# Kernel tuning notes

Measured on AMD Instinct MI355X. Metric: run time of the kernel, lower is better.

The kernel has to match this reference:

```python
import jax, jax.numpy as jnp
import numpy as np

B, T = 128, 512
IN, Z, H, E, TR = 88, 80, 400, 100, 200


def setup_inputs() -> dict:
    key = jax.random.key(0)
    ks = jax.random.split(key, 16)
    r = lambda i, shape: (0.05 * jax.random.normal(ks[i], shape)).astype(jnp.float32)
    z32 = lambda n: jnp.zeros((n,), dtype=jnp.float32)
    return dict(
        mini_batch=jax.random.uniform(ks[0], (B, T, IN), dtype=jnp.float32),
        eps=jax.random.normal(ks[1], (B, T, Z), dtype=jnp.float32),
        W_ih=r(2, (H, IN)), W_hh=r(3, (H, H)), b_ih=z32(H), b_hh=z32(H),
        h0=z32(H), z0=z32(Z),
        W_loc=r(4, (Z, H)), b_loc=z32(Z), W_scale=r(5, (Z, H)), b_scale=z32(Z),
        gW1=r(6, (TR, Z)), gb1=z32(TR), gW2=r(7, (Z, TR)), gb2=z32(Z),
        pW1=r(8, (TR, Z)), pb1=z32(TR), pW2=r(9, (Z, TR)), pb2=z32(Z),
        sW=r(10, (Z, Z)), sb=z32(Z),
        lW=jnp.eye(Z, dtype=jnp.float32), lb=z32(Z),  # lin_z_to_loc initialized to identity in torch code
        eW1=r(11, (E, Z)), eb1=z32(E), eW2=r(12, (E, E)), eb2=z32(E),
        eW3=r(13, (IN, E)), eb3=z32(IN),
    )


def reference(mini_batch, eps, W_ih, W_hh, b_ih, b_hh, h0, z0,
              W_loc, b_loc, W_scale, b_scale,
              gW1, gb1, gW2, gb2, pW1, pb1, pW2, pb2, sW, sb, lW, lb,
              eW1, eb1, eW2, eb2, eW3, eb3):
    Bb = mini_batch.shape[0]
    # --- guide: Elman RNN (relu) over time-reversed input, then reverse back ---
    xr = mini_batch[:, ::-1, :]                          # [B,T,IN]
    pre = jnp.einsum('bti,hi->bth', xr, W_ih) + b_ih     # [B,T,H] input projection precomputed

    def step(h, p):                                      # h:[B,H], p:[B,H]
        h = jax.nn.relu(p + h @ W_hh.T + b_hh)
        return h, h

    h_init = jnp.broadcast_to(h0, (Bb, h0.shape[0]))
    _, hs = jax.lax.scan(step, h_init, jnp.swapaxes(pre, 0, 1))  # hs:[T,B,H]
    rnn_out = jnp.swapaxes(hs, 0, 1)[:, ::-1, :]         # pad_and_reverse (full-length seqs)

    # --- Combiner (meanfield): q(z_t) params, reparameterized sample ---
    z_loc = rnn_out @ W_loc.T + b_loc                    # [B,T,Z]
    z_scale = jax.nn.softplus(rnn_out @ W_scale.T + b_scale)
    z = z_loc + z_scale * eps                            # rsample

    # --- model: GatedTransition on shifted z ---
    z_shift = jnp.concatenate([jnp.broadcast_to(z0, (Bb, 1, z0.shape[0])), z[:, :-1]], axis=1)
    gate = jax.nn.sigmoid(jax.nn.relu(z_shift @ gW1.T + gb1) @ gW2.T + gb2)
    prop = jax.nn.relu(z_shift @ pW1.T + pb1) @ pW2.T + pb2
    trans_loc = (1.0 - gate) * (z_shift @ lW.T + lb) + gate * prop
    trans_scale = jax.nn.softplus(jax.nn.relu(prop) @ sW.T + sb)

    # --- Emitter: p(x_t | z_t) ---
    h1 = jax.nn.relu(z @ eW1.T + eb1)
    h2 = jax.nn.relu(h1 @ eW2.T + eb2)
    emis = jax.nn.sigmoid(h2 @ eW3.T + eb3)              # [B,T,IN]

    return jnp.concatenate([emis, trans_loc, trans_scale], axis=-1)  # [B,T,IN+2Z]
```

## Files before the change

### kernel.cpp

```cpp
#include <hip/hip_runtime.h>
#include <math.h>

typedef unsigned int uint;

constexpr int BB  = 128;
constexpr int TT  = 512;
constexpr int DIN = 88;
constexpr int DZ  = 80;
constexpr int DH  = 400;
constexpr int DE  = 100;
constexpr int DTR = 200;
constexpr int DOUT = DIN + DZ + DZ;

typedef __attribute__((ext_vector_type(8))) short bf16x8;
typedef __attribute__((ext_vector_type(4))) float f32x4;
union FU { uint4 u; bf16x8 v; };

__device__ __forceinline__ float softplusf(float x) {
    return fmaxf(x, 0.f) + log1pf(__expf(-fabsf(x)));
}
__device__ __forceinline__ float sigmoidf(float x) {
    return 1.f / (1.f + __expf(-x));
}
__device__ __forceinline__ uint bf16rn(float f) {
    uint u = __float_as_uint(f);
    return (u + 0x7FFFu + ((u >> 16) & 1u)) >> 16;
}
__device__ __forceinline__ uint pk2(float lo, float hi) {
    return bf16rn(lo) | (bf16rn(hi) << 16);
}
#define DOT2(ACC, Wv, Hv) asm("v_dot2_f32_bf16 %0, %1, %2, %0" : "+v"(ACC) : "v"(Wv), "v"(Hv))

__device__ __forceinline__ bf16x8 fragF32(const float* p) {
    float4 f0 = *(const float4*)p, f1 = *(const float4*)(p + 4);
    FU fu;
    fu.u.x = pk2(f0.x, f0.y); fu.u.y = pk2(f0.z, f0.w);
    fu.u.z = pk2(f1.x, f1.y); fu.u.w = pk2(f1.z, f1.w);
    return fu.v;
}
__device__ __forceinline__ bf16x8 fragF32relu(const float* p) {
    float4 f0 = *(const float4*)p, f1 = *(const float4*)(p + 4);
    FU fu;
    fu.u.x = pk2(fmaxf(f0.x, 0.f), fmaxf(f0.y, 0.f));
    fu.u.y = pk2(fmaxf(f0.z, 0.f), fmaxf(f0.w, 0.f));
    fu.u.z = pk2(fmaxf(f1.x, 0.f), fmaxf(f1.y, 0.f));
    fu.u.w = pk2(fmaxf(f1.z, 0.f), fmaxf(f1.w, 0.f));
    return fu.v;
}
#define MFMA(A, B, C) __builtin_amdgcn_mfma_f32_16x16x32_bf16((A), (B), (C), 0, 0, 0)


__global__ void packb_kernel(const float* __restrict__ W, uint* __restrict__ dst,
                             int O, int K, int KS, int tileOff) {
    int tile = blockIdx.x, r = threadIdx.x;
    int l = r >> 2, d = r & 3;
    int nt = tile / KS, ks = tile % KS;
    int o = nt * 16 + (l & 15);
    int k = ks * 32 + ((l >> 4) << 3) + 2 * d;
    uint lo = 0, hi = 0;
    if (o < O && k < K)     lo = bf16rn(W[o * K + k]);
    if (o < O && k + 1 < K) hi = bf16rn(W[o * K + k + 1]);
    dst[(size_t)(tileOff + tile) * 256 + r] = lo | (hi << 16);
}

__global__ void pack_rnn(const float* __restrict__ W_hh, uint* __restrict__ Wb) {
    int idx = blockIdx.x * 256 + threadIdx.x;
    if (idx >= 200 * 512) return;
    int t = idx & 511, j = idx >> 9;
    uint val = 0u;
    int p = -1, hf = 0;
    if (t < 200) { p = t; hf = 0; }
    else if (t >= 256 && t < 456) { p = t - 256; hf = 1; }
    if (p >= 0) {
        int r  = 2 * p + (j >= 100 ? 1 : 0);
        int kd = hf * 100 + (j % 100);
        val = pk2(W_hh[r * DH + 2 * kd], W_hh[r * DH + 2 * kd + 1]);
    }
    Wb[(j >> 2) * 2048 + t * 4 + (j & 3)] = val;
}

__global__ __launch_bounds__(256) void pre_kernel(
    const float* __restrict__ x, const uint* __restrict__ bt,
    const float* __restrict__ b_ih, const float* __restrict__ b_hh,
    float* __restrict__ pre) {
    __shared__ float xs[16 * 100];
    const int b = blockIdx.y, tt0 = blockIdx.x * 16, tid = threadIdx.x;
    const int l = tid & 63, wid = tid >> 6, lr = l & 15, lg = l >> 4;
    for (int idx = tid; idx < 1600; idx += 256) {
        int r = idx / 100, k = idx % 100;
        xs[idx] = (k < DIN) ? x[((size_t)b * TT + (TT - 1 - (tt0 + r))) * DIN + k] : 0.f;
    }
    __syncthreads();
    bf16x8 af[3];
    #pragma unroll
    for (int ks = 0; ks < 3; ++ks) af[ks] = fragF32(xs + lr * 100 + ks * 32 + lg * 8);
    const uint4* bt4 = (const uint4*)bt;
    for (int nt = wid; nt < 25; nt += 4) {
        f32x4 acc = {0.f, 0.f, 0.f, 0.f};
        const uint4* bp = bt4 + (size_t)(388 + nt * 3) * 64 + l;
        #pragma unroll
        for (int ks = 0; ks < 3; ++ks) { FU bu; bu.u = bp[ks * 64]; acc = MFMA(af[ks], bu.v, acc); }
        int col = nt * 16 + lr;
        float bias = b_ih[col] + b_hh[col];
        #pragma unroll
        for (int i = 0; i < 4; ++i)
            pre[((size_t)b * TT + tt0 + lg * 4 + i) * DH + col] = acc[i] + bias;
    }
}

#define DLOOP(OFF)                                                              \
    _Pragma("unroll")                                                           \
    for (int d = 0; d < 100; ++d) {                                             \
        const int kd = (OFF) + d;                                               \
        const int hsrc = ((kd >> 6) == 0) ? hl0 : ((kd >> 6) == 1) ? hl1        \
                        : ((kd >> 6) == 2) ? hl2 : hl3;                         \
        int hv = __builtin_amdgcn_readlane(hsrc, kd & 63);                      \
        if (d & 1) { DOT2(r0b, W[d], hv); DOT2(r1b, W[100 + d], hv); }          \
        else       { DOT2(r0a, W[d], hv); DOT2(r1a, W[100 + d], hv); }          \
    }

__global__ __launch_bounds__(512) __attribute__((amdgpu_waves_per_eu(2, 2)))
void rnn_kernel(const uint* __restrict__ Wb, const float* __restrict__ h0,
                float* hs) {
    __shared__ uint h_lds[256];
    __shared__ float2 part[200];

    const int tid = threadIdx.x;
    const int lane = tid & 63;
    const bool a0 = (tid < 200);
    const bool a1 = (tid >= 256) && (tid < 456);
    const int p = a0 ? tid : (a1 ? tid - 256 : 0);

    uint W[200];
    const uint4* Wb4 = (const uint4*)Wb;
    #pragma unroll
    for (int j4 = 0; j4 < 50; ++j4) {
        uint4 v = Wb4[j4 * 512 + tid];
        W[4 * j4 + 0] = v.x; W[4 * j4 + 1] = v.y;
        W[4 * j4 + 2] = v.z; W[4 * j4 + 3] = v.w;
    }
    #pragma unroll
    for (int j = 0; j < 200; ++j) asm volatile("" : "+v"(W[j]));

    if (tid < 256)
        h_lds[tid] = (tid < 200) ? pk2(h0[2 * tid], h0[2 * tid + 1]) : 0u;
    __syncthreads();

    float* base = hs + (size_t)blockIdx.x * TT * DH;
    float2 pcur = make_float2(0.f, 0.f);
    if (a0) pcur = *(const float2*)(base + 2 * p);

    for (int tt = 0; tt < TT; ++tt) {
        int hl0 = (int)h_lds[lane];
        int hl1 = (int)h_lds[64 + lane];
        int hl2 = (int)h_lds[128 + lane];
        int hl3 = (int)h_lds[192 + lane];

        float2 pnxt = make_float2(0.f, 0.f);
        if (a0 && tt + 1 < TT) pnxt = *(const float2*)(base + (size_t)(tt + 1) * DH + 2 * p);

        float r0a = 0.f, r0b = 0.f, r1a = 0.f, r1b = 0.f;
        if (a0)      { DLOOP(0) }
        else if (a1) { DLOOP(100) }

        if (a1) part[p] = make_float2(r0a + r0b, r1a + r1b);
        __syncthreads();
        if (a0) {
            float2 q = part[p];
            float v0 = fmaxf(pcur.x + r0a + r0b + q.x, 0.f);
            float v1 = fmaxf(pcur.y + r1a + r1b + q.y, 0.f);
            uint pkd = pk2(v0, v1);
            h_lds[p] = pkd;
            ((uint*)(base + (size_t)tt * DH))[p] = pkd;
            pcur = pnxt;
        }
        __syncthreads();
    }
}

__global__ __launch_bounds__(256) void e_kernel(
    const uint4* __restrict__ hs4, const float* __restrict__ eps,
    const float* __restrict__ z0, const uint* __restrict__ bt,
    const float* __restrict__ b_loc, const float* __restrict__ b_scale,
    const float* __restrict__ gb1, const float* __restrict__ pb1,
    const float* __restrict__ gb2, const float* __restrict__ pb2,
    const float* __restrict__ lb,  const float* __restrict__ sb,
    const float* __restrict__ eb1, const float* __restrict__ eb2,
    const float* __restrict__ eb3, float* __restrict__ out) {
    __shared__ float lds[12196];
    float* zl = lds;
    float* AP = lds + 1700;
    float* gp = lds + 8996;

    const int tid = threadIdx.x, l = tid & 63, wid = tid >> 6;
    const int b = blockIdx.y, t0 = blockIdx.x * 16;
    const int lr = l & 15, lg = l >> 4;
    const uint4* bt4 = (const uint4*)bt;

    bf16x8 zf[3];

    {
        const int m0 = (wid >> 1) * 16;
        int r = m0 + lr;
        int t = t0 - 1 + r; t = min(max(t, 0), TT - 1);
        const uint4* rp = hs4 + ((size_t)b * TT + (TT - 1 - t)) * 100;
        bf16x8 af[13];
        FU zz; zz.u = make_uint4(0u, 0u, 0u, 0u);
        #pragma unroll
        for (int ks = 0; ks < 13; ++ks) {
            if (ks == 12 && lg >= 2) af[ks] = zz.v;
            else { FU fu; fu.u = rp[ks * 4 + lg]; af[ks] = fu.v; }
        }
        for (int nt = (wid & 1); nt < 10; nt += 2) {
            f32x4 acc = {0.f, 0.f, 0.f, 0.f};
            const uint4* bp = bt4 + (size_t)(nt * 13) * 64 + l;
            #pragma unroll
            for (int ks = 0; ks < 13; ++ks) { FU bu; bu.u = bp[ks * 64]; acc = MFMA(af[ks], bu.v, acc); }
            int col = nt * 16 + lr;
            float bias = (col < DZ) ? b_loc[col] : b_scale[col - DZ];
            #pragma unroll
            for (int i = 0; i < 4; ++i) {
                int rr = m0 + lg * 4 + i;
                if (rr < 17) AP[rr * 164 + col] = acc[i] + bias;
            }
        }
    }
    __syncthreads();

    for (int idx = tid; idx < 17 * 100; idx += 256) {
        int r = idx / 100, o = idx % 100;
        float zv = 0.f;
        if (o < DZ) {
            int t = t0 - 1 + r;
            if (t < 0) zv = z0[o];
            else {
                float sp = softplusf(AP[r * 164 + DZ + o]);
                zv = AP[r * 164 + o] + sp * eps[((size_t)b * TT + t) * DZ + o];
            }
        }
        zl[idx] = zv;
    }
    __syncthreads();

    {
        #pragma unroll
        for (int ks = 0; ks < 3; ++ks) zf[ks] = fragF32(zl + lr * 100 + ks * 32 + lg * 8);
        for (int idx = tid; idx < 640; idx += 256) {
            int h = idx / 320, rem = idx % 320;
            AP[h * 3648 + (rem / 20) * 228 + 208 + rem % 20] = 0.f;
        }
        for (int nt = wid; nt < 26; nt += 4) {
            f32x4 acc = {0.f, 0.f, 0.f, 0.f};
            const uint4* bp = bt4 + (size_t)(130 + nt * 3) * 64 + l;
            #pragma unroll
            for (int ks = 0; ks < 3; ++ks) { FU bu; bu.u = bp[ks * 64]; acc = MFMA(zf[ks], bu.v, acc); }
            int isP = nt >= 13;
            int col = (isP ? nt - 13 : nt) * 16 + lr;
            float bias = (col < DTR) ? (isP ? pb1[col] : gb1[col]) : 0.f;
            float* dst = AP + isP * 3648;
            #pragma unroll
            for (int i = 0; i < 4; ++i)
                dst[(lg * 4 + i) * 228 + col] = fmaxf(acc[i] + bias, 0.f);
        }
    }
    __syncthreads();

    {
        int half = wid >> 1;
        const float* src = AP + half * 3648;
        bf16x8 apf[7];
        #pragma unroll
        for (int ks = 0; ks < 7; ++ks) apf[ks] = fragF32(src + lr * 228 + ks * 32 + lg * 8);
        for (int idx = tid; idx < 640; idx += 256) {
            int h = idx / 320, rem = idx % 320;
            gp[h * 1600 + (rem / 20) * 100 + 80 + rem % 20] = 0.f;
        }
        for (int nt = (wid & 1); nt < 5; nt += 2) {
            f32x4 acc = {0.f, 0.f, 0.f, 0.f};
            const uint4* bp = bt4 + (size_t)(208 + half * 35 + nt * 7) * 64 + l;
            #pragma unroll
            for (int ks = 0; ks < 7; ++ks) { FU bu; bu.u = bp[ks * 64]; acc = MFMA(apf[ks], bu.v, acc); }
            int col = nt * 16 + lr;
            float bias = half ? pb2[col] : gb2[col];
            float* dst = gp + half * 1600;
            #pragma unroll
            for (int i = 0; i < 4; ++i) {
                float v = acc[i] + bias;
                dst[(lg * 4 + i) * 100 + col] = half ? v : sigmoidf(v);
            }
        }
    }
    __syncthreads();

    {
        bf16x8 z1f[3], prf[3];
        #pragma unroll
        for (int ks = 0; ks < 3; ++ks) {
            z1f[ks] = fragF32(zl + (1 + lr) * 100 + ks * 32 + lg * 8);
            prf[ks] = fragF32relu(gp + 1600 + lr * 100 + ks * 32 + lg * 8);
        }
        for (int tsk = wid; tsk < 18; tsk += 4) {
            if (tsk < 5) {
                f32x4 acc = {0.f, 0.f, 0.f, 0.f};
                const uint4* bp = bt4 + (size_t)(278 + tsk * 3) * 64 + l;
                #pragma unroll
                for (int ks = 0; ks < 3; ++ks) { FU bu; bu.u = bp[ks * 64]; acc = MFMA(zf[ks], bu.v, acc); }
                int col = tsk * 16 + lr;
                float bias = lb[col];
                #pragma unroll
                for (int i = 0; i < 4; ++i) {
                    int rr = lg * 4 + i;
                    float g  = gp[rr * 100 + col];
                    float pv = gp[1600 + rr * 100 + col];
                    out[((size_t)b * TT + t0 + rr) * DOUT + DIN + col] =
                        (1.f - g) * (acc[i] + bias) + g * pv;
                }
            } else if (tsk < 10) {
                int nt = tsk - 5;
                f32x4 acc = {0.f, 0.f, 0.f, 0.f};
                const uint4* bp = bt4 + (size_t)(293 + nt * 3) * 64 + l;
                #pragma unroll
                for (int ks = 0; ks < 3; ++ks) { FU bu; bu.u = bp[ks * 64]; acc = MFMA(prf[ks], bu.v, acc); }
                int col = nt * 16 + lr;
                float bias = sb[col];
                #pragma unroll
                for (int i = 0; i < 4; ++i)
                    out[((size_t)b * TT + t0 + lg * 4 + i) * DOUT + DIN + DZ + col] =
                        softplusf(acc[i] + bias);
            } else {
                int nt = tsk - 10;
                f32x4 acc = {0.f, 0.f, 0.f, 0.f};
                const uint4* bp = bt4 + (size_t)(308 + nt * 3) * 64 + l;
                #pragma unroll
                for (int ks = 0; ks < 3; ++ks) { FU bu; bu.u = bp[ks * 64]; acc = MFMA(z1f[ks], bu.v, acc); }
                int col = nt * 16 + lr;
                float bias = (col < DE) ? eb1[col] : 0.f;
                #pragma unroll
                for (int i = 0; i < 4; ++i)
                    AP[(lg * 4 + i) * 228 + col] = fmaxf(acc[i] + bias, 0.f);
            }
        }
    }
    __syncthreads();

    {
        bf16x8 hf[4];
        #pragma unroll
        for (int ks = 0; ks < 4; ++ks) hf[ks] = fragF32(AP + lr * 228 + ks * 32 + lg * 8);
        for (int nt = wid; nt < 8; nt += 4) {
            f32x4 acc = {0.f, 0.f, 0.f, 0.f};
            const uint4* bp = bt4 + (size_t)(332 + nt * 4) * 64 + l;
            #pragma unroll
            for (int ks = 0; ks < 4; ++ks) { FU bu; bu.u = bp[ks * 64]; acc = MFMA(hf[ks], bu.v, acc); }
            int col = nt * 16 + lr;
            float bias = (col < DE) ? eb2[col] : 0.f;
            #pragma unroll
            for (int i = 0; i < 4; ++i)
                AP[3648 + (lg * 4 + i) * 228 + col] = fmaxf(acc[i] + bias, 0.f);
        }
    }
    __syncthreads();

    {
        bf16x8 hf[4];
        #pragma unroll
        for (int ks = 0; ks < 4; ++ks) hf[ks] = fragF32(AP + 3648 + lr * 228 + ks * 32 + lg * 8);
        for (int nt = wid; nt < 6; nt += 4) {
            f32x4 acc = {0.f, 0.f, 0.f, 0.f};
            const uint4* bp = bt4 + (size_t)(364 + nt * 4) * 64 + l;
            #pragma unroll
            for (int ks = 0; ks < 4; ++ks) { FU bu; bu.u = bp[ks * 64]; acc = MFMA(hf[ks], bu.v, acc); }
            int col = nt * 16 + lr;
            if (col < DIN) {
                float bias = eb3[col];
                #pragma unroll
                for (int i = 0; i < 4; ++i)
                    out[((size_t)b * TT + t0 + lg * 4 + i) * DOUT + col] = sigmoidf(acc[i] + bias);
            }
        }
    }
}

extern "C" void kernel_launch(void* const* d_in, const int* in_sizes, int n_in,
                              void* d_out, int out_size, void* d_ws, size_t ws_size,
                              hipStream_t stream) {
    const float* x       = (const float*)d_in[0];
    const float* eps     = (const float*)d_in[1];
    const float* W_ih    = (const float*)d_in[2];
    const float* W_hh    = (const float*)d_in[3];
    const float* b_ih    = (const float*)d_in[4];
    const float* b_hh    = (const float*)d_in[5];
    const float* h0      = (const float*)d_in[6];
    const float* z0      = (const float*)d_in[7];
    const float* W_loc   = (const float*)d_in[8];
    const float* b_loc   = (const float*)d_in[9];
    const float* W_scale = (const float*)d_in[10];
    const float* b_scale = (const float*)d_in[11];
    const float* gW1 = (const float*)d_in[12];
    const float* gb1 = (const float*)d_in[13];
    const float* gW2 = (const float*)d_in[14];
    const float* gb2 = (const float*)d_in[15];
    const float* pW1 = (const float*)d_in[16];
    const float* pb1 = (const float*)d_in[17];
    const float* pW2 = (const float*)d_in[18];
    const float* pb2 = (const float*)d_in[19];
    const float* sW  = (const float*)d_in[20];
    const float* sb  = (const float*)d_in[21];
    const float* lW  = (const float*)d_in[22];
    const float* lb  = (const float*)d_in[23];
    const float* eW1 = (const float*)d_in[24];
    const float* eb1 = (const float*)d_in[25];
    const float* eW2 = (const float*)d_in[26];
    const float* eb2 = (const float*)d_in[27];
    const float* eW3 = (const float*)d_in[28];
    const float* eb3 = (const float*)d_in[29];

    float* wsf = (float*)d_ws;
    float* prebuf = wsf;
    uint*  Wb = (uint*)(wsf + (size_t)BB * TT * DH);
    uint*  bt = Wb + 102400;

    pack_rnn<<<400, 256, 0, stream>>>(W_hh, Wb);
    packb_kernel<<<5 * 13, 256, 0, stream>>>(W_loc,   bt,  DZ, DH, 13, 0);
    packb_kernel<<<5 * 13, 256, 0, stream>>>(W_scale, bt,  DZ, DH, 13, 65);
    packb_kernel<<<13 * 3, 256, 0, stream>>>(gW1,     bt, DTR, DZ,  3, 130);
    packb_kernel<<<13 * 3, 256, 0, stream>>>(pW1,     bt, DTR, DZ,  3, 169);
    packb_kernel<<<5 * 7,  256, 0, stream>>>(gW2,     bt,  DZ, DTR, 7, 208);
    packb_kernel<<<5 * 7,  256, 0, stream>>>(pW2,     bt,  DZ, DTR, 7, 243);
    packb_kernel<<<5 * 3,  256, 0, stream>>>(lW,      bt,  DZ, DZ,  3, 278);
    packb_kernel<<<5 * 3,  256, 0, stream>>>(sW,      bt,  DZ, DZ,  3, 293);
    packb_kernel<<<8 * 3,  256, 0, stream>>>(eW1,     bt,  DE, DZ,  3, 308);
    packb_kernel<<<8 * 4,  256, 0, stream>>>(eW2,     bt,  DE, DE,  4, 332);
    packb_kernel<<<6 * 4,  256, 0, stream>>>(eW3,     bt, DIN, DE,  4, 364);
    packb_kernel<<<25 * 3, 256, 0, stream>>>(W_ih,    bt,  DH, DIN, 3, 388);

    pre_kernel<<<dim3(TT / 16, BB), 256, 0, stream>>>(x, bt, b_ih, b_hh, prebuf);
    rnn_kernel<<<dim3(BB), dim3(512), 0, stream>>>(Wb, h0, prebuf);
    e_kernel<<<dim3(TT / 16, BB), 256, 0, stream>>>(
        (const uint4*)prebuf, eps, z0, bt,
        b_loc, b_scale, gb1, pb1, gb2, pb2, lb, sb, eb1, eb2, eb3,
        (float*)d_out);
}
```

Before: 1.172 ms.

## Batch 16 sequences per block in RNN recurrence using MFMA instead of dot2

The RNN recurrence previously ran one block per sequence (128 blocks), with each thread doing scalar bf16 dot2 products against register-resident W_hh rows. It now runs 8 blocks of 16 sequences each. W_hh is held as MFMA A-fragments in registers, plus one tile in LDS, and the 16 hidden states are multiplied with 16x16x32 bf16 MFMAs each step. Hidden state and pre-activations are double-buffered in LDS so there is one barrier per step, and all weight-packing launches are merged into a single kernel. The trade-off is only 8 CUs active on a serial chain, with heavier register pressure and per-step LDS traffic.

```diff
diff --git a/kernel.cpp b/kernel.cpp
--- a/kernel.cpp
+++ b/kernel.cpp
@@ -14,7 +14,8 @@
 
 typedef __attribute__((ext_vector_type(8))) short bf16x8;
 typedef __attribute__((ext_vector_type(4))) float f32x4;
-union FU { uint4 u; bf16x8 v; };
+typedef __attribute__((ext_vector_type(4))) uint  u32x4;
+union FU { u32x4 u; bf16x8 v; };
 
 __device__ __forceinline__ float softplusf(float x) {
     return fmaxf(x, 0.f) + log1pf(__expf(-fabsf(x)));
@@ -29,8 +30,6 @@
 __device__ __forceinline__ uint pk2(float lo, float hi) {
     return bf16rn(lo) | (bf16rn(hi) << 16);
 }
-#define DOT2(ACC, Wv, Hv) asm("v_dot2_f32_bf16 %0, %1, %2, %0" : "+v"(ACC) : "v"(Wv), "v"(Hv))
-
 __device__ __forceinline__ bf16x8 fragF32(const float* p) {
     float4 f0 = *(const float4*)p, f1 = *(const float4*)(p + 4);
     FU fu;
@@ -49,35 +48,30 @@
 }
 #define MFMA(A, B, C) __builtin_amdgcn_mfma_f32_16x16x32_bf16((A), (B), (C), 0, 0, 0)
 
-
-__global__ void packb_kernel(const float* __restrict__ W, uint* __restrict__ dst,
-                             int O, int K, int KS, int tileOff) {
-    int tile = blockIdx.x, r = threadIdx.x;
-    int l = r >> 2, d = r & 3;
-    int nt = tile / KS, ks = tile % KS;
+struct Srcs { const float* p[13]; };
+
+__global__ __launch_bounds__(256) void packall_kernel(Srcs s, uint* __restrict__ dst) {
+    constexpr int O_[13]   = {80,80,200,200,80,80,80,80,100,100,88,400,400};
+    constexpr int K_[13]   = {400,400,80,80,200,200,80,80,80,100,100,88,400};
+    constexpr int KS_[13]  = {13,13,3,3,7,7,3,3,3,4,4,3,13};
+    constexpr int OFF_[13] = {0,65,130,169,208,243,278,293,308,332,364,388,463};
+    int tile = blockIdx.x;
+    int e = 0;
+    #pragma unroll
+    for (int i = 1; i < 13; ++i) if (tile >= OFF_[i]) e = i;
+    int lt = tile - OFF_[e];
+    int nt = lt / KS_[e], ks = lt % KS_[e];
+    const float* W = s.p[e];
+    int r = threadIdx.x, l = r >> 2, d = r & 3;
     int o = nt * 16 + (l & 15);
     int k = ks * 32 + ((l >> 4) << 3) + 2 * d;
     uint lo = 0, hi = 0;
-    if (o < O && k < K)     lo = bf16rn(W[o * K + k]);
-    if (o < O && k + 1 < K) hi = bf16rn(W[o * K + k + 1]);
-    dst[(size_t)(tileOff + tile) * 256 + r] = lo | (hi << 16);
-}
-
-__global__ void pack_rnn(const float* __restrict__ W_hh, uint* __restrict__ Wb) {
-    int idx = blockIdx.x * 256 + threadIdx.x;
-    if (idx >= 200 * 512) return;
-    int t = idx & 511, j = idx >> 9;
-    uint val = 0u;
-    int p = -1, hf = 0;
-    if (t < 200) { p = t; hf = 0; }
-    else if (t >= 256 && t < 456) { p = t - 256; hf = 1; }
-    if (p >= 0) {
-        int r  = 2 * p + (j >= 100 ? 1 : 0);
-        int kd = hf * 100 + (j % 100);
-        val = pk2(W_hh[r * DH + 2 * kd], W_hh[r * DH + 2 * kd + 1]);
-    }
-    Wb[(j >> 2) * 2048 + t * 4 + (j & 3)] = val;
-}
+    if (o < O_[e] && k < K_[e])     lo = bf16rn(W[o * K_[e] + k]);
+    if (o < O_[e] && k + 1 < K_[e]) hi = bf16rn(W[o * K_[e] + k + 1]);
+    dst[(size_t)tile * 256 + r] = lo | (hi << 16);
+}
+
+constexpr int WHH = 463;
 
 __global__ __launch_bounds__(256) void pre_kernel(
     const float* __restrict__ x, const uint* __restrict__ bt,
@@ -99,7 +93,7 @@
         f32x4 acc = {0.f, 0.f, 0.f, 0.f};
         const uint4* bp = bt4 + (size_t)(388 + nt * 3) * 64 + l;
         #pragma unroll
-        for (int ks = 0; ks < 3; ++ks) { FU bu; bu.u = bp[ks * 64]; acc = MFMA(af[ks], bu.v, acc); }
+        for (int ks = 0; ks < 3; ++ks) { FU bu; bu.u = *(const u32x4*)(bp + ks * 64); acc = MFMA(af[ks], bu.v, acc); }
         int col = nt * 16 + lr;
         float bias = b_ih[col] + b_hh[col];
         #pragma unroll
@@ -108,73 +102,110 @@
     }
 }
 
-#define DLOOP(OFF)                                                              \
-    _Pragma("unroll")                                                           \
-    for (int d = 0; d < 100; ++d) {                                             \
-        const int kd = (OFF) + d;                                               \
-        const int hsrc = ((kd >> 6) == 0) ? hl0 : ((kd >> 6) == 1) ? hl1        \
-                        : ((kd >> 6) == 2) ? hl2 : hl3;                         \
-        int hv = __builtin_amdgcn_readlane(hsrc, kd & 63);                      \
-        if (d & 1) { DOT2(r0b, W[d], hv); DOT2(r1b, W[100 + d], hv); }          \
-        else       { DOT2(r0a, W[d], hv); DOT2(r1a, W[100 + d], hv); }          \
-    }
-
 __global__ __launch_bounds__(512) __attribute__((amdgpu_waves_per_eu(2, 2)))
-void rnn_kernel(const uint* __restrict__ Wb, const float* __restrict__ h0,
-                float* hs) {
-    __shared__ uint h_lds[256];
-    __shared__ float2 part[200];
-
-    const int tid = threadIdx.x;
-    const int lane = tid & 63;
-    const bool a0 = (tid < 200);
-    const bool a1 = (tid >= 256) && (tid < 456);
-    const int p = a0 ? tid : (a1 ? tid - 256 : 0);
-
-    uint W[200];
-    const uint4* Wb4 = (const uint4*)Wb;
+void rnn_kernel(const u32x4* __restrict__ bt4, const float* __restrict__ h0,
+                float* __restrict__ prehs) {
+    extern __shared__ char smem[];
+    uint*  hb   = (uint*)smem;
+    float* pb   = (float*)(smem + 27136);
+    u32x4* wt24 = (u32x4*)(smem + 27136 + 51712);
+
+    const int tid = threadIdx.x, lane = tid & 63, wid = tid >> 6;
+    const int batch = lane & 15, lg = lane >> 4;
+    const int b0 = blockIdx.x * 16;
+
+    u32x4 A0[13], A1[13], A2[13];
+    {
+        const u32x4* base = bt4 + (size_t)(WHH + 3 * wid * 13) * 64 + lane;
+        #pragma unroll
+        for (int ks = 0; ks < 13; ++ks) {
+            A0[ks] = base[ks * 64];
+            A1[ks] = base[(13 + ks) * 64];
+            A2[ks] = base[(26 + ks) * 64];
+        }
+    }
     #pragma unroll
-    for (int j4 = 0; j4 < 50; ++j4) {
-        uint4 v = Wb4[j4 * 512 + tid];
-        W[4 * j4 + 0] = v.x; W[4 * j4 + 1] = v.y;
-        W[4 * j4 + 2] = v.z; W[4 * j4 + 3] = v.w;
-    }
-    #pragma unroll
-    for (int j = 0; j < 200; ++j) asm volatile("" : "+v"(W[j]));
-
-    if (tid < 256)
-        h_lds[tid] = (tid < 200) ? pk2(h0[2 * tid], h0[2 * tid + 1]) : 0u;
-    __syncthreads();
-
-    float* base = hs + (size_t)blockIdx.x * TT * DH;
-    float2 pcur = make_float2(0.f, 0.f);
-    if (a0) pcur = *(const float2*)(base + 2 * p);
-
+    for (int ks = 0; ks < 13; ++ks)
+        asm volatile("" : "+v"(A0[ks]), "+v"(A1[ks]), "+v"(A2[ks]));
+
+    for (int i = tid; i < 13 * 64; i += 512)
+        wt24[i] = bt4[(size_t)(WHH + 24 * 13) * 64 + i];
+
+    for (int i = tid; i < 2 * 16 * 12; i += 512) {
+        int buf = i / 192, r = i % 192, bs = r / 12, d = 200 + r % 12;
+        hb[buf * 3392 + bs * 212 + d] = 0u;
+    }
+    for (int i = tid; i < 16 * 200; i += 512) {
+        int bs = i / 200, d = i % 200;
+        hb[bs * 212 + d] = pk2(h0[2 * d], h0[2 * d + 1]);
+    }
+    {
+        const u32x4* ra = (const u32x4*)(prehs + ((size_t)(b0 + 2 * wid) * TT) * DH);
+        const u32x4* rb = (const u32x4*)(prehs + ((size_t)(b0 + 2 * wid + 1) * TT) * DH);
+        u32x4* wa = (u32x4*)(pb + (2 * wid) * 404);
+        u32x4* wb = (u32x4*)(pb + (2 * wid + 1) * 404);
+        wa[lane] = ra[lane];
+        wb[lane] = rb[lane];
+        if (lane < 36) { wa[64 + lane] = ra[64 + lane]; wb[64 + lane] = rb[64 + lane]; }
+    }
+    __syncthreads();
+
+    uint cur = 0;
     for (int tt = 0; tt < TT; ++tt) {
-        int hl0 = (int)h_lds[lane];
-        int hl1 = (int)h_lds[64 + lane];
-        int hl2 = (int)h_lds[128 + lane];
-        int hl3 = (int)h_lds[192 + lane];
-
-        float2 pnxt = make_float2(0.f, 0.f);
-        if (a0 && tt + 1 < TT) pnxt = *(const float2*)(base + (size_t)(tt + 1) * DH + 2 * p);
-
-        float r0a = 0.f, r0b = 0.f, r1a = 0.f, r1b = 0.f;
-        if (a0)      { DLOOP(0) }
-        else if (a1) { DLOOP(100) }
-
-        if (a1) part[p] = make_float2(r0a + r0b, r1a + r1b);
+        u32x4 na0, na1, nb0, nb1;
+        const bool hasNext = (tt + 1 < TT);
+        if (hasNext) {
+            const u32x4* ra = (const u32x4*)(prehs + ((size_t)(b0 + 2 * wid) * TT + tt + 1) * DH);
+            const u32x4* rb = (const u32x4*)(prehs + ((size_t)(b0 + 2 * wid + 1) * TT + tt + 1) * DH);
+            na0 = ra[lane]; nb0 = rb[lane];
+            if (lane < 36) { na1 = ra[64 + lane]; nb1 = rb[64 + lane]; }
+        }
+
+        const uint*  hcur = hb + cur * 3392;
+        const float* pcur = pb + cur * (16 * 404);
+        f32x4 c0 = {0.f, 0.f, 0.f, 0.f}, c1 = c0, c2 = c0, c24 = c0;
+        const u32x4* hrow = (const u32x4*)(hcur + batch * 212);
+        #pragma unroll
+        for (int ks = 0; ks < 13; ++ks) {
+            FU b; b.u = hrow[ks * 4 + lg];
+            FU a0; a0.u = A0[ks]; c0 = MFMA(a0.v, b.v, c0);
+            FU a1; a1.u = A1[ks]; c1 = MFMA(a1.v, b.v, c1);
+            FU a2; a2.u = A2[ks]; c2 = MFMA(a2.v, b.v, c2);
+            if (wid == 7) { FU w; w.u = wt24[ks * 64 + lane]; c24 = MFMA(w.v, b.v, c24); }
+        }
+
+        uint*  hnxt = hb + (cur ^ 1) * 3392;
+        float* pnxt = pb + (cur ^ 1) * (16 * 404);
+        uint*  grow = (uint*)prehs + ((size_t)(b0 + batch) * TT + tt) * DH;
+
+        #pragma unroll
+        for (int s = 0; s < 3; ++s) {
+            const int mt = 3 * wid + s;
+            f32x4 c = (s == 0) ? c0 : (s == 1) ? c1 : c2;
+            float4 pr = *(const float4*)(pcur + batch * 404 + mt * 16 + lg * 4);
+            uint d0 = pk2(fmaxf(c[0] + pr.x, 0.f), fmaxf(c[1] + pr.y, 0.f));
+            uint d1 = pk2(fmaxf(c[2] + pr.z, 0.f), fmaxf(c[3] + pr.w, 0.f));
+            uint2 dd = make_uint2(d0, d1);
+            *(uint2*)(hnxt + batch * 212 + mt * 8 + lg * 2) = dd;
+            *(uint2*)(grow + mt * 8 + lg * 2) = dd;
+        }
+        if (wid == 7) {
+            float4 pr = *(const float4*)(pcur + batch * 404 + 24 * 16 + lg * 4);
+            uint d0 = pk2(fmaxf(c24[0] + pr.x, 0.f), fmaxf(c24[1] + pr.y, 0.f));
+            uint d1 = pk2(fmaxf(c24[2] + pr.z, 0.f), fmaxf(c24[3] + pr.w, 0.f));
+            uint2 dd = make_uint2(d0, d1);
+            *(uint2*)(hnxt + batch * 212 + 24 * 8 + lg * 2) = dd;
+            *(uint2*)(grow + 24 * 8 + lg * 2) = dd;
+        }
+
+        if (hasNext) {
+            u32x4* wa = (u32x4*)(pnxt + (2 * wid) * 404);
+            u32x4* wb = (u32x4*)(pnxt + (2 * wid + 1) * 404);
+            wa[lane] = na0; wb[lane] = nb0;
+            if (lane < 36) { wa[64 + lane] = na1; wb[64 + lane] = nb1; }
+        }
         __syncthreads();
-        if (a0) {
-            float2 q = part[p];
-            float v0 = fmaxf(pcur.x + r0a + r0b + q.x, 0.f);
-            float v1 = fmaxf(pcur.y + r1a + r1b + q.y, 0.f);
-            uint pkd = pk2(v0, v1);
-            h_lds[p] = pkd;
-            ((uint*)(base + (size_t)tt * DH))[p] = pkd;
-            pcur = pnxt;
-        }
-        __syncthreads();
+        cur ^= 1;
     }
 }
 
@@ -205,17 +236,17 @@
         int t = t0 - 1 + r; t = min(max(t, 0), TT - 1);
         const uint4* rp = hs4 + ((size_t)b * TT + (TT - 1 - t)) * 100;
         bf16x8 af[13];
-        FU zz; zz.u = make_uint4(0u, 0u, 0u, 0u);
+        FU zz; zz.u = (u32x4){0u, 0u, 0u, 0u};
         #pragma unroll
         for (int ks = 0; ks < 13; ++ks) {
             if (ks == 12 && lg >= 2) af[ks] = zz.v;
-            else { FU fu; fu.u = rp[ks * 4 + lg]; af[ks] = fu.v; }
+            else { FU fu; fu.u = *(const u32x4*)(rp + ks * 4 + lg); af[ks] = fu.v; }
         }
         for (int nt = (wid & 1); nt < 10; nt += 2) {
             f32x4 acc = {0.f, 0.f, 0.f, 0.f};
             const uint4* bp = bt4 + (size_t)(nt * 13) * 64 + l;
             #pragma unroll
-            for (int ks = 0; ks < 13; ++ks) { FU bu; bu.u = bp[ks * 64]; acc = MFMA(af[ks], bu.v, acc); }
+            for (int ks = 0; ks < 13; ++ks) { FU bu; bu.u = *(const u32x4*)(bp + ks * 64); acc = MFMA(af[ks], bu.v, acc); }
             int col = nt * 16 + lr;
             float bias = (col < DZ) ? b_loc[col] : b_scale[col - DZ];
             #pragma unroll
@@ -253,7 +284,7 @@
             f32x4 acc = {0.f, 0.f, 0.f, 0.f};
             const uint4* bp = bt4 + (size_t)(130 + nt * 3) * 64 + l;
             #pragma unroll
-            for (int ks = 0; ks < 3; ++ks) { FU bu; bu.u = bp[ks * 64]; acc = MFMA(zf[ks], bu.v, acc); }
+            for (int ks = 0; ks < 3; ++ks) { FU bu; bu.u = *(const u32x4*)(bp + ks * 64); acc = MFMA(zf[ks], bu.v, acc); }
             int isP = nt >= 13;
             int col = (isP ? nt - 13 : nt) * 16 + lr;
             float bias = (col < DTR) ? (isP ? pb1[col] : gb1[col]) : 0.f;
@@ -279,7 +310,7 @@
             f32x4 acc = {0.f, 0.f, 0.f, 0.f};
             const uint4* bp = bt4 + (size_t)(208 + half * 35 + nt * 7) * 64 + l;
             #pragma unroll
-            for (int ks = 0; ks < 7; ++ks) { FU bu; bu.u = bp[ks * 64]; acc = MFMA(apf[ks], bu.v, acc); }
+            for (int ks = 0; ks < 7; ++ks) { FU bu; bu.u = *(const u32x4*)(bp + ks * 64); acc = MFMA(apf[ks], bu.v, acc); }
             int col = nt * 16 + lr;
             float bias = half ? pb2[col] : gb2[col];
             float* dst = gp + half * 1600;
@@ -304,7 +335,7 @@
                 f32x4 acc = {0.f, 0.f, 0.f, 0.f};
                 const uint4* bp = bt4 + (size_t)(278 + tsk * 3) * 64 + l;
                 #pragma unroll
-                for (int ks = 0; ks < 3; ++ks) { FU bu; bu.u = bp[ks * 64]; acc = MFMA(zf[ks], bu.v, acc); }
+                for (int ks = 0; ks < 3; ++ks) { FU bu; bu.u = *(const u32x4*)(bp + ks * 64); acc = MFMA(zf[ks], bu.v, acc); }
                 int col = tsk * 16 + lr;
                 float bias = lb[col];
                 #pragma unroll
@@ -320,7 +351,7 @@
                 f32x4 acc = {0.f, 0.f, 0.f, 0.f};
                 const uint4* bp = bt4 + (size_t)(293 + nt * 3) * 64 + l;
                 #pragma unroll
-                for (int ks = 0; ks < 3; ++ks) { FU bu; bu.u = bp[ks * 64]; acc = MFMA(prf[ks], bu.v, acc); }
+                for (int ks = 0; ks < 3; ++ks) { FU bu; bu.u = *(const u32x4*)(bp + ks * 64); acc = MFMA(prf[ks], bu.v, acc); }
                 int col = nt * 16 + lr;
                 float bias = sb[col];
                 #pragma unroll
@@ -332,7 +363,7 @@
                 f32x4 acc = {0.f, 0.f, 0.f, 0.f};
                 const uint4* bp = bt4 + (size_t)(308 + nt * 3) * 64 + l;
                 #pragma unroll
-                for (int ks = 0; ks < 3; ++ks) { FU bu; bu.u = bp[ks * 64]; acc = MFMA(z1f[ks], bu.v, acc); }
+                for (int ks = 0; ks < 3; ++ks) { FU bu; bu.u = *(const u32x4*)(bp + ks * 64); acc = MFMA(z1f[ks], bu.v, acc); }
                 int col = nt * 16 + lr;
                 float bias = (col < DE) ? eb1[col] : 0.f;
                 #pragma unroll
@@ -351,7 +382,7 @@
             f32x4 acc = {0.f, 0.f, 0.f, 0.f};
             const uint4* bp = bt4 + (size_t)(332 + nt * 4) * 64 + l;
             #pragma unroll
-            for (int ks = 0; ks < 4; ++ks) { FU bu; bu.u = bp[ks * 64]; acc = MFMA(hf[ks], bu.v, acc); }
+            for (int ks = 0; ks < 4; ++ks) { FU bu; bu.u = *(const u32x4*)(bp + ks * 64); acc = MFMA(hf[ks], bu.v, acc); }
             int col = nt * 16 + lr;
             float bias = (col < DE) ? eb2[col] : 0.f;
             #pragma unroll
@@ -369,7 +400,7 @@
             f32x4 acc = {0.f, 0.f, 0.f, 0.f};
             const uint4* bp = bt4 + (size_t)(364 + nt * 4) * 64 + l;
             #pragma unroll
-            for (int ks = 0; ks < 4; ++ks) { FU bu; bu.u = bp[ks * 64]; acc = MFMA(hf[ks], bu.v, acc); }
+            for (int ks = 0; ks < 4; ++ks) { FU bu; bu.u = *(const u32x4*)(bp + ks * 64); acc = MFMA(hf[ks], bu.v, acc); }
             int col = nt * 16 + lr;
             if (col < DIN) {
                 float bias = eb3[col];
@@ -417,25 +448,21 @@
 
     float* wsf = (float*)d_ws;
     float* prebuf = wsf;
-    uint*  Wb = (uint*)(wsf + (size_t)BB * TT * DH);
-    uint*  bt = Wb + 102400;
-
-    pack_rnn<<<400, 256, 0, stream>>>(W_hh, Wb);
-    packb_kernel<<<5 * 13, 256, 0, stream>>>(W_loc,   bt,  DZ, DH, 13, 0);
-    packb_kernel<<<5 * 13, 256, 0, stream>>>(W_scale, bt,  DZ, DH, 13, 65);
-    packb_kernel<<<13 * 3, 256, 0, stream>>>(gW1,     bt, DTR, DZ,  3, 130);
-    packb_kernel<<<13 * 3, 256, 0, stream>>>(pW1,     bt, DTR, DZ,  3, 169);
-    packb_kernel<<<5 * 7,  256, 0, stream>>>(gW2,     bt,  DZ, DTR, 7, 208);
-    packb_kernel<<<5 * 7,  256, 0, stream>>>(pW2,     bt,  DZ, DTR, 7, 243);
-    packb_kernel<<<5 * 3,  256, 0, stream>>>(lW,      bt,  DZ, DZ,  3, 278);
-    packb_kernel<<<5 * 3,  256, 0, stream>>>(sW,      bt,  DZ, DZ,  3, 293);
-    packb_kernel<<<8 * 3,  256, 0, stream>>>(eW1,     bt,  DE, DZ,  3, 308);
-    packb_kernel<<<8 * 4,  256, 0, stream>>>(eW2,     bt,  DE, DE,  4, 332);
-    packb_kernel<<<6 * 4,  256, 0, stream>>>(eW3,     bt, DIN, DE,  4, 364);
-    packb_kernel<<<25 * 3, 256, 0, stream>>>(W_ih,    bt,  DH, DIN, 3, 388);
+    uint*  bt = (uint*)(wsf + (size_t)BB * TT * DH);
+
+    Srcs s;
+    s.p[0] = W_loc;  s.p[1] = W_scale; s.p[2] = gW1; s.p[3] = pW1;
+    s.p[4] = gW2;    s.p[5] = pW2;     s.p[6] = lW;  s.p[7] = sW;
+    s.p[8] = eW1;    s.p[9] = eW2;     s.p[10] = eW3; s.p[11] = W_ih; s.p[12] = W_hh;
+    packall_kernel<<<788, 256, 0, stream>>>(s, bt);
 
     pre_kernel<<<dim3(TT / 16, BB), 256, 0, stream>>>(x, bt, b_ih, b_hh, prebuf);
-    rnn_kernel<<<dim3(BB), dim3(512), 0, stream>>>(Wb, h0, prebuf);
+
+    size_t smem = 27136 + 51712 + 13312;
+    hipFuncSetAttribute((const void*)rnn_kernel,
+                        hipFuncAttributeMaxDynamicSharedMemorySize, (int)smem);
+    rnn_kernel<<<dim3(8), dim3(512), smem, stream>>>((const u32x4*)bt, h0, prebuf);
+
     e_kernel<<<dim3(TT / 16, BB), 256, 0, stream>>>(
         (const uint4*)prebuf, eps, z0, bt,
         b_loc, b_scale, gb1, pb1, gb2, pb2, lb, sb, eb1, eb2, eb3,
```

Result: faster. 1.130 ms (-3.6%).
